# Optimization experiments

Hardware: AMD Instinct MI355X
Metric: run time of the kernel (lower is better)

The kernel has to match this reference:

```python
import jax, jax.numpy as jnp
import numpy as np

N_USERS = 60000
N_ITEMS = 40000
D = 64
N_BEH = 3
L_GLOBAL = 2
L_SINGLE = 2
E_GLOBAL = 1_000_000
E_BEH = 500_000
BATCH = 4096
REG_WEIGHT = 1e-3
DIM_QK = 64
N_NODES = N_USERS + 1 + N_ITEMS + 1
USER_GLOBAL_W = 2.35
USER_BEH_W = 0.242
ITEM_GLOBAL_W = 1.0
ITEM_BEH_W = 0.55


def setup_inputs() -> dict:
    key = jax.random.key(0)
    ks = jax.random.split(key, 9)
    user_emb = (jax.random.normal(ks[0], (N_USERS + 1, D), jnp.float32) * 0.1).at[0].set(0.0)
    item_emb = (jax.random.normal(ks[1], (N_ITEMS + 1, D), jnp.float32) * 0.1).at[0].set(0.0)
    w_scale = 1.0 / np.sqrt(D)
    global_W = jax.random.normal(ks[2], (L_GLOBAL, D, D), jnp.float32) * w_scale
    global_b = jnp.zeros((L_GLOBAL, D), jnp.float32)
    beh_W = jax.random.normal(ks[3], (N_BEH, L_SINGLE, D, D), jnp.float32) * w_scale
    beh_b = jnp.zeros((N_BEH, L_SINGLE, D), jnp.float32)
    all_edge_index = jax.random.randint(ks[4], (2, E_GLOBAL), 0, N_NODES, jnp.int32)
    beh_edge_index = jax.random.randint(ks[5], (N_BEH, 2, E_BEH), 0, N_NODES, jnp.int32)
    batch_data = jax.random.randint(ks[6], (BATCH, N_BEH, 3), 0, N_ITEMS + 1, jnp.int32)
    return {
        "user_emb": user_emb, "item_emb": item_emb,
        "global_W": global_W, "global_b": global_b,
        "beh_W": beh_W, "beh_b": beh_b,
        "all_edge_index": all_edge_index, "beh_edge_index": beh_edge_index,
        "batch_data": batch_data,
    }


def _gcn_conv(h, src, dst, W, b):
    # PyG GCNConv, add_self_loops=False: out[dst] += d^-1/2[src] d^-1/2[dst] (h W)[src] + b
    N = h.shape[0]
    hw = h @ W
    deg = jnp.zeros((N,), hw.dtype).at[dst].add(1.0)
    dinv = jnp.where(deg > 0, jax.lax.rsqrt(jnp.maximum(deg, 1.0)), 0.0)
    coef = (dinv[src] * dinv[dst])[:, None]          # [E,1]
    out = jax.ops.segment_sum(hw[src] * coef, dst, num_segments=N)
    return out + b


def _graph_encoder(x, edge_index, Ws, bs):
    src, dst = edge_index[0], edge_index[1]
    res = x
    h = x
    for i in range(Ws.shape[0]):
        h = _gcn_conv(h, src, dst, Ws[i], bs[i])
        h = h / jnp.maximum(jnp.linalg.norm(h, axis=-1, keepdims=True), 1e-12)  # F.normalize
        res = res + h / (i + 1.0)
    return res


def _mutual_attention(tok):
    # tok: [N, B, D]; per-node BxB softmax attention
    scale = 1.0 / np.sqrt(DIM_QK)
    att = jax.nn.softmax(jnp.einsum('nbd,ncd->nbc', tok, tok) * scale, axis=-1)
    return jnp.einsum('nbc,ncd->nbd', att, tok)


def reference(user_emb, item_emb, global_W, global_b, beh_W, beh_b,
              all_edge_index, beh_edge_index, batch_data):
    nu = user_emb.shape[0]
    all_emb = jnp.concatenate([user_emb, item_emb], axis=0)        # [N, D]
    all_emb = _graph_encoder(all_emb, all_edge_index, global_W, global_b)
    u_g, i_g = all_emb[:nu], all_emb[nu:]
    beh_u, beh_i = [], []
    for b_idx in range(N_BEH):
        e = _graph_encoder(all_emb, beh_edge_index[b_idx], beh_W[b_idx], beh_b[b_idx])
        beh_u.append(e[:nu])
        beh_i.append(e[nu:])
    all_u = jnp.stack(beh_u, axis=1)                               # [nu, B, D]
    all_i = jnp.stack(beh_i, axis=1)                               # [ni, B, D]
    all_u = _mutual_attention(all_u)
    all_i = _mutual_attention(all_i)
    uw = USER_GLOBAL_W * u_g[:, None, :] + USER_BEH_W * all_u      # [nu, B, D]
    iw = ITEM_GLOBAL_W * i_g[:, None, :] + ITEM_BEH_W * all_i      # [ni, B, D]

    total = jnp.float32(0.0)
    for i in range(N_BEH):
        data = batch_data[:, i]
        users = data[:, 0]
        items = data[:, 1:]                                        # [batch, 2]
        uf = uw[:, i][users][:, None, :]                           # [batch, 1, D]
        for j in range(N_BEH):
            itf = iw[:, j][items]                                  # [batch, 2, D]
            scores = jnp.sum(uf * itf, axis=2)                     # [batch, 2]
            total = total - jnp.mean(jax.nn.log_sigmoid(scores[:, 0] - scores[:, 1]))
    emb_loss = (jnp.linalg.norm(user_emb) + jnp.linalg.norm(item_emb)) / item_emb.shape[0]
    return total + REG_WEIGHT * emb_loss
```

## Files before the change

kernel.cpp:

```cpp
#include <hip/hip_runtime.h>
#include <math.h>

#define NU 60001
#define NI 40001
#define NN 100002
#define EG 1000000
#define EB 500000
#define BATCH 4096
#define NPASS 4
#define PASSW 25001
#define EC 36
#define SENTB (NN * 64)

typedef float floatx2 __attribute__((ext_vector_type(2)));
typedef short bf16x8 __attribute__((ext_vector_type(8)));
typedef float f32x4 __attribute__((ext_vector_type(4)));

__device__ inline float wave_sum(float v) {
#pragma unroll
  for (int off = 32; off > 0; off >>= 1) v += __shfl_down(v, off);
  return __shfl(v, 0);
}

__device__ inline float sub_sum16(float v) {
#pragma unroll
  for (int off = 8; off > 0; off >>= 1) v += __shfl_xor(v, off);
  return v;
}

__device__ inline float dot4(float4 a, float4 b) {
  return fmaf(a.x, b.x, fmaf(a.y, b.y, fmaf(a.z, b.z, a.w * b.w)));
}

__device__ inline unsigned short f2b(float f) {
  unsigned u = __float_as_uint(f);
  return (unsigned short)((u + 0x7fffu + ((u >> 16) & 1u)) >> 16);
}
__device__ inline float b2f(unsigned short h) {
  return __uint_as_float((unsigned)h << 16);
}
__device__ inline float4 ld4b(const unsigned short* p) {
  ushort4 u = *(const ushort4*)p;
  return make_float4(b2f(u.x), b2f(u.y), b2f(u.z), b2f(u.w));
}
__device__ inline unsigned pack2b(float a, float b) {
  return (unsigned)f2b(a) | ((unsigned)f2b(b) << 16);
}

__device__ inline unsigned char f2fp8(float f) {
  return (unsigned char)(__builtin_amdgcn_cvt_pk_fp8_f32(f, f, 0, false) & 0xff);
}
__device__ inline unsigned int pack4_fp8(float4 v) {
  int pk = __builtin_amdgcn_cvt_pk_fp8_f32(v.x, v.y, 0, false);
  pk = __builtin_amdgcn_cvt_pk_fp8_f32(v.z, v.w, pk, true);
  return (unsigned int)pk;
}

__global__ void k_bucket(const int* __restrict__ eg, const int* __restrict__ eb,
                         int* __restrict__ cnt, int* __restrict__ edg,
                         int lo, int hi) {
  int set = blockIdx.y;
  int E = set ? EB : EG;
  int e = blockIdx.x * blockDim.x + threadIdx.x;
  if (e >= E) return;
  const int* sp = set ? (eb + (long)(set - 1) * 2 * EB) : eg;
  int d = sp[E + e];
  if (d < lo || d >= hi) return;
  int s = sp[e];
  int pos = atomicAdd(cnt + set * NN + d, 1);
  if (pos < EC) edg[((long)set * NN + d) * EC + pos] = s << 6;
}

__global__ void k_dinv(const int* __restrict__ cnt, float* __restrict__ dinv) {
  int i = blockIdx.x * blockDim.x + threadIdx.x;
  if (i < 4 * NN) {
    int c = cnt[i];
    dinv[i] = (c > 0) ? rsqrtf((float)c) : 0.f;
  }
}

__global__ void k_zsent(unsigned char* __restrict__ tbsb, unsigned char* __restrict__ asg,
                        unsigned char* __restrict__ asb) {
  const long NEp = (long)(NN + 1) * 64;
  int t = threadIdx.x;
  int row = t >> 6, b = t & 63;
  if (row < 3) tbsb[row * NEp + SENTB + b] = 0;
  else if (row == 3) asg[SENTB + b] = 0;
  else if (row < 7) asb[(row - 4) * NEp + SENTB + b] = 0;
}

__global__ void k_tbs0(const float4* __restrict__ ue, const float4* __restrict__ ie,
                       const float* __restrict__ dinv, unsigned int* __restrict__ out) {
  long i = (long)blockIdx.x * blockDim.x + threadIdx.x;
  if (i >= (long)(NN + 1) * 16) return;
  int row = (int)(i >> 4);
  if (row >= NN) { out[i] = 0; return; }
  float4 v = (row < NU) ? ue[i] : ie[i - (long)NU * 16];
  float dv = dinv[row];
  v.x *= dv; v.y *= dv; v.z *= dv; v.w *= dv;
  out[i] = pack4_fp8(v);
}

template <int MODE>
__global__ void __launch_bounds__(256) k_gcn(
    const unsigned char* __restrict__ tb, const int* __restrict__ edg,
    const int* __restrict__ cnt, const float* __restrict__ dinv,
    const float* __restrict__ Wb, const float* __restrict__ biasb,
    const float* __restrict__ basef, const float* __restrict__ base2f,
    const unsigned short* __restrict__ base16,
    unsigned short* __restrict__ res16, unsigned char* __restrict__ outS,
    unsigned char* __restrict__ tbs123) {
  __shared__ __align__(16) short accs[32][72];
  __shared__ float ssq[32][2];
  const long NE = (long)NN * 64;
  const long NEp = (long)(NN + 1) * 64;

  int t = threadIdx.x;
  int w = t >> 6, lane = t & 63;
  int sub3 = lane >> 3, sl8 = lane & 7;
  int sub = lane >> 4, sl16 = lane & 15;
  int set = blockIdx.y;

  const float *W, *bias;
  if (MODE <= 1) { W = Wb; bias = biasb; }
  else {
    W = Wb + (long)set * 8192 + (MODE == 3 ? 4096 : 0);
    bias = biasb + set * 128 + (MODE == 3 ? 64 : 0);
  }
  int cs = (MODE >= 2) ? (1 + set) : 0;
  const unsigned char* tbl = (MODE >= 2) ? tb + (long)set * NEp : tb;
  unsigned char* outp = (MODE == 2) ? outS + (long)set * NEp : outS;

  int tilebase = (w >> 1) << 4;
  int cg = (w & 1) << 5;
  int ncolA = cg + sl16, ncolB = cg + 16 + sl16;
  bf16x8 bfA0, bfA1, bfB0, bfB1;
#pragma unroll
  for (int j = 0; j < 8; j++) {
    int k0 = (sub * 8 + j) * 64, k1 = (32 + sub * 8 + j) * 64;
    bfA0[j] = (short)f2b(W[k0 + ncolA]);
    bfA1[j] = (short)f2b(W[k1 + ncolA]);
    bfB0[j] = (short)f2b(W[k0 + ncolB]);
    bfB1[j] = (short)f2b(W[k1 + ncolB]);
  }
  float biasA = bias[ncolA], biasB = bias[ncolB];

  int nb0 = blockIdx.x * 32;
  int node = nb0 + (w << 3) + sub3;
  floatx2 a0 = {0.f, 0.f}, a1 = {0.f, 0.f}, a2 = {0.f, 0.f}, a3 = {0.f, 0.f};
  int deg = 0;
  float dvn = 0.f;
  const int* ep = edg;
  if (node < NN) {
    deg = min(cnt[cs * NN + node], EC);
    dvn = dinv[cs * NN + node];
    ep = edg + ((long)cs * NN + node) * EC;
  }
  int mx = deg;
  mx = max(mx, __shfl_xor(mx, 8));
  mx = max(mx, __shfl_xor(mx, 16));
  mx = max(mx, __shfl_xor(mx, 32));
  int lb = lane & 56;
  for (int ch = 0; ch < mx; ch += 8) {
    int rem = deg - ch;
    int e = (sl8 < rem) ? ep[ch + sl8] : 0;
#pragma unroll
    for (int i = 0; i < 8; i += 4) {
      int s0 = __shfl(e, lb + i),     s1 = __shfl(e, lb + i + 1);
      int s2 = __shfl(e, lb + i + 2), s3 = __shfl(e, lb + i + 3);
      int o0 = (i + 0 < rem) ? s0 : SENTB;
      int o1 = (i + 1 < rem) ? s1 : SENTB;
      int o2 = (i + 2 < rem) ? s2 : SENTB;
      int o3 = (i + 3 < rem) ? s3 : SENTB;
      uint2 r0 = *(const uint2*)(tbl + o0 + (sl8 << 3));
      uint2 r1 = *(const uint2*)(tbl + o1 + (sl8 << 3));
      uint2 r2 = *(const uint2*)(tbl + o2 + (sl8 << 3));
      uint2 r3 = *(const uint2*)(tbl + o3 + (sl8 << 3));
      a0 += __builtin_amdgcn_cvt_pk_f32_fp8(r0.x, false);
      a1 += __builtin_amdgcn_cvt_pk_f32_fp8(r0.x, true);
      a2 += __builtin_amdgcn_cvt_pk_f32_fp8(r0.y, false);
      a3 += __builtin_amdgcn_cvt_pk_f32_fp8(r0.y, true);
      a0 += __builtin_amdgcn_cvt_pk_f32_fp8(r1.x, false);
      a1 += __builtin_amdgcn_cvt_pk_f32_fp8(r1.x, true);
      a2 += __builtin_amdgcn_cvt_pk_f32_fp8(r1.y, false);
      a3 += __builtin_amdgcn_cvt_pk_f32_fp8(r1.y, true);
      a0 += __builtin_amdgcn_cvt_pk_f32_fp8(r2.x, false);
      a1 += __builtin_amdgcn_cvt_pk_f32_fp8(r2.x, true);
      a2 += __builtin_amdgcn_cvt_pk_f32_fp8(r2.y, false);
      a3 += __builtin_amdgcn_cvt_pk_f32_fp8(r2.y, true);
      a0 += __builtin_amdgcn_cvt_pk_f32_fp8(r3.x, false);
      a1 += __builtin_amdgcn_cvt_pk_f32_fp8(r3.x, true);
      a2 += __builtin_amdgcn_cvt_pk_f32_fp8(r3.y, false);
      a3 += __builtin_amdgcn_cvt_pk_f32_fp8(r3.y, true);
    }
  }
  floatx2 dv2 = {dvn, dvn};
  a0 *= dv2; a1 *= dv2; a2 *= dv2; a3 *= dv2;
  int4 pk4;
  pk4.x = (int)pack2b(a0.x, a0.y);
  pk4.y = (int)pack2b(a1.x, a1.y);
  pk4.z = (int)pack2b(a2.x, a2.y);
  pk4.w = (int)pack2b(a3.x, a3.y);
  *(int4*)&accs[(w << 3) + sub3][sl8 << 3] = pk4;
  __syncthreads();

  int arow = tilebase + sl16;
  bf16x8 fa0 = *(const bf16x8*)&accs[arow][sub << 3];
  bf16x8 fa1 = *(const bf16x8*)&accs[arow][32 + (sub << 3)];
  f32x4 cA = {0.f, 0.f, 0.f, 0.f}, cB = {0.f, 0.f, 0.f, 0.f};
  cA = __builtin_amdgcn_mfma_f32_16x16x32_bf16(fa0, bfA0, cA, 0, 0, 0);
  cA = __builtin_amdgcn_mfma_f32_16x16x32_bf16(fa1, bfA1, cA, 0, 0, 0);
  cB = __builtin_amdgcn_mfma_f32_16x16x32_bf16(fa0, bfB0, cB, 0, 0, 0);
  cB = __builtin_amdgcn_mfma_f32_16x16x32_bf16(fa1, bfB1, cB, 0, 0, 0);

  float vA[4], vB[4];
#pragma unroll
  for (int r = 0; r < 4; r++) { vA[r] = cA[r] + biasA; vB[r] = cB[r] + biasB; }
#pragma unroll
  for (int r = 0; r < 4; r++) {
    float p = sub_sum16(fmaf(vA[r], vA[r], vB[r] * vB[r]));
    if (sl16 == 0) ssq[tilebase + (sub << 2) + r][w & 1] = p;
  }
  __syncthreads();
#pragma unroll
  for (int r = 0; r < 4; r++) {
    int nl = tilebase + (sub << 2) + r;
    float ss = ssq[nl][0] + ssq[nl][1];
    float inv = 1.0f / fmaxf(sqrtf(ss), 1e-12f);
    float hA = vA[r] * inv, hB = vB[r] * inv;
    int gn = nb0 + nl;
    if (gn < NN) {
      long iA = (long)gn * 64 + ncolA, iB = (long)gn * 64 + ncolB;
      float dv = dinv[cs * NN + gn];
      if (MODE == 0 || MODE == 2) {
        outp[iA] = f2fp8(hA * dv);
        outp[iB] = f2fp8(hB * dv);
      } else if (MODE == 1) {
        float idv = (dv > 0.f) ? 1.0f / dv : 0.f;
        float ownA = __builtin_amdgcn_cvt_f32_fp8((unsigned int)tbl[iA], 0) * idv;
        float ownB = __builtin_amdgcn_cvt_f32_fp8((unsigned int)tbl[iB], 0) * idv;
        float bA, bB;
        if (gn < NU) { bA = basef[iA]; bB = basef[iB]; }
        else {
          long o2 = (long)(gn - NU) * 64;
          bA = base2f[o2 + ncolA]; bB = base2f[o2 + ncolB];
        }
        float rA = bA + ownA + 0.5f * hA, rB = bB + ownB + 0.5f * hB;
        res16[iA] = f2b(rA); res16[iB] = f2b(rB);
#pragma unroll
        for (int k = 0; k < 3; k++) {
          float dk = dinv[(1 + k) * NN + gn];
          tbs123[(long)k * NEp + iA] = f2fp8(rA * dk);
          tbs123[(long)k * NEp + iB] = f2fp8(rB * dk);
        }
      } else {
        float idv = (dv > 0.f) ? 1.0f / dv : 0.f;
        float ownA = __builtin_amdgcn_cvt_f32_fp8((unsigned int)tbl[iA], 0) * idv;
        float ownB = __builtin_amdgcn_cvt_f32_fp8((unsigned int)tbl[iB], 0) * idv;
        float rA = b2f(base16[iA]) + ownA + 0.5f * hA;
        float rB = b2f(base16[iB]) + ownB + 0.5f * hB;
        (res16 + (long)set * NE)[iA] = f2b(rA);
        (res16 + (long)set * NE)[iB] = f2b(rB);
      }
    }
  }
}

__device__ inline void item_iw4(const unsigned short* __restrict__ G,
                                const unsigned short* __restrict__ B0,
                                const unsigned short* __restrict__ B1,
                                const unsigned short* __restrict__ B2,
                                long o, float4& iw0, float4& iw1, float4& iw2) {
  float4 g = ld4b(G + o);
  float4 t0 = ld4b(B0 + o);
  float4 t1 = ld4b(B1 + o);
  float4 t2 = ld4b(B2 + o);
  float g00 = sub_sum16(dot4(t0, t0)), g01 = sub_sum16(dot4(t0, t1));
  float g02 = sub_sum16(dot4(t0, t2)), g11 = sub_sum16(dot4(t1, t1));
  float g12 = sub_sum16(dot4(t1, t2)), g22 = sub_sum16(dot4(t2, t2));
  const float S = 0.125f;
  float gm[3][3] = {{g00, g01, g02}, {g01, g11, g12}, {g02, g12, g22}};
  float4* out[3] = {&iw0, &iw1, &iw2};
#pragma unroll
  for (int j = 0; j < 3; j++) {
    float a0 = gm[j][0] * S, a1 = gm[j][1] * S, a2 = gm[j][2] * S;
    float m = fmaxf(a0, fmaxf(a1, a2));
    float e0 = expf(a0 - m), e1 = expf(a1 - m), e2 = expf(a2 - m);
    float inv = 1.f / (e0 + e1 + e2);
    float w0 = e0 * inv, w1 = e1 * inv, w2 = e2 * inv;
    float4 r;
    r.x = fmaf(0.55f, w0 * t0.x + w1 * t1.x + w2 * t2.x, g.x);
    r.y = fmaf(0.55f, w0 * t0.y + w1 * t1.y + w2 * t2.y, g.y);
    r.z = fmaf(0.55f, w0 * t0.z + w1 * t1.z + w2 * t2.z, g.z);
    r.w = fmaf(0.55f, w0 * t0.w + w1 * t1.w + w2 * t2.w, g.w);
    *out[j] = r;
  }
}

__global__ void __launch_bounds__(256) k_loss(
    const unsigned short* __restrict__ G, const unsigned short* __restrict__ B0,
    const unsigned short* __restrict__ B1, const unsigned short* __restrict__ B2,
    const int* __restrict__ batch, float* __restrict__ acc) {
  int tid = blockIdx.x * blockDim.x + threadIdx.x;
  int lane = tid & 63;
  int sub = lane >> 4, sl = lane & 15;
  int task = (tid >> 6) * 4 + sub;
  if (task >= BATCH * 3) return;
  int i = task % 3;
  const int* bd = batch + (long)task * 3;
  int u = bd[0], p = bd[1], q = bd[2];

  float4 uf;
  {
    long o = (long)u * 64 + sl * 4;
    float4 g = ld4b(G + o);
    float4 t0 = ld4b(B0 + o);
    float4 t1 = ld4b(B1 + o);
    float4 t2 = ld4b(B2 + o);
    float4 ti = (i == 0) ? t0 : ((i == 1) ? t1 : t2);
    float a0 = sub_sum16(dot4(ti, t0)) * 0.125f;
    float a1 = sub_sum16(dot4(ti, t1)) * 0.125f;
    float a2 = sub_sum16(dot4(ti, t2)) * 0.125f;
    float m = fmaxf(a0, fmaxf(a1, a2));
    float e0 = expf(a0 - m), e1 = expf(a1 - m), e2 = expf(a2 - m);
    float inv = 1.f / (e0 + e1 + e2);
    float w0 = e0 * inv, w1 = e1 * inv, w2 = e2 * inv;
    uf.x = fmaf(2.35f, g.x, 0.242f * (w0 * t0.x + w1 * t1.x + w2 * t2.x));
    uf.y = fmaf(2.35f, g.y, 0.242f * (w0 * t0.y + w1 * t1.y + w2 * t2.y));
    uf.z = fmaf(2.35f, g.z, 0.242f * (w0 * t0.z + w1 * t1.z + w2 * t2.z));
    uf.w = fmaf(2.35f, g.w, 0.242f * (w0 * t0.w + w1 * t1.w + w2 * t2.w));
  }

  float4 p0, p1, p2, q0, q1, q2;
  item_iw4(G, B0, B1, B2, ((long)(NU + p)) * 64 + sl * 4, p0, p1, p2);
  item_iw4(G, B0, B1, B2, ((long)(NU + q)) * 64 + sl * 4, q0, q1, q2);

  float sp0 = sub_sum16(dot4(uf, p0)), sq0 = sub_sum16(dot4(uf, q0));
  float sp1 = sub_sum16(dot4(uf, p1)), sq1 = sub_sum16(dot4(uf, q1));
  float sp2 = sub_sum16(dot4(uf, p2)), sq2 = sub_sum16(dot4(uf, q2));

  if (sl == 0) {
    float loc = 0.f;
    float xs[3] = {sp0 - sq0, sp1 - sq1, sp2 - sq2};
#pragma unroll
    for (int j = 0; j < 3; j++) {
      float x = xs[j];
      loc += fminf(x, 0.f) - log1pf(expf(-fabsf(x)));
    }
    atomicAdd(acc, loc);
  }
}

__global__ void k_sumsq(const float* __restrict__ x, long n, float* __restrict__ acc) {
  long stride = (long)gridDim.x * blockDim.x;
  float v = 0.f;
  for (long i = (long)blockIdx.x * blockDim.x + threadIdx.x; i < n; i += stride) {
    float t = x[i];
    v = fmaf(t, t, v);
  }
  v = wave_sum(v);
  if ((threadIdx.x & 63) == 0) atomicAdd(acc, v);
}

__global__ void k_final(const float* __restrict__ acc, float* __restrict__ out) {
  out[0] = -acc[0] * (1.0f / (float)BATCH) +
           0.001f * ((sqrtf(acc[1]) + sqrtf(acc[2])) / (float)NI);
}

extern "C" void kernel_launch(void* const* d_in, const int* in_sizes, int n_in,
                              void* d_out, int out_size, void* d_ws, size_t ws_size,
                              hipStream_t stream) {
  const float* ue = (const float*)d_in[0];
  const float* ie = (const float*)d_in[1];
  const float* gW = (const float*)d_in[2];
  const float* gb = (const float*)d_in[3];
  const float* bW = (const float*)d_in[4];
  const float* bb = (const float*)d_in[5];
  const int* eg = (const int*)d_in[6];
  const int* eb = (const int*)d_in[7];
  const int* batch = (const int*)d_in[8];
  float* out = (float*)d_out;

  const long NE = (long)NN * 64;
  const long NEp = (long)(NN + 1) * 64;
  unsigned short* G16 = (unsigned short*)d_ws;
  unsigned short* B16 = G16 + NE;
  float* DINV = (float*)(B16 + 3 * NE);
  float* ACC = DINV + 4 * NN;
  int* CNT = (int*)(ACC + 8);
  int* EDG = CNT + 4 * NN;
  unsigned char* TBS0 = (unsigned char*)(EDG + 4L * NN * EC);
  unsigned char* TBSb = TBS0 + NEp;
  unsigned char* ASg = TBSb + 3 * NEp;
  unsigned char* ASb = ASg + NEp;

  hipMemsetAsync(ACC, 0, 8 * sizeof(float), stream);
  hipMemsetAsync(CNT, 0, 4 * NN * sizeof(int), stream);

  const int GB = (NN + 31) / 32;

  dim3 ge((EG + 255) / 256, 4);

  for (int p = 0; p < NPASS; p++)
    k_bucket<<<ge, 256, 0, stream>>>(eg, eb, CNT, EDG,
                                     p * PASSW, min(NN, (p + 1) * PASSW));
  k_dinv<<<(4 * NN + 255) / 256, 256, 0, stream>>>(CNT, DINV);
  k_zsent<<<1, 512, 0, stream>>>(TBSb, ASg, ASb);
  k_tbs0<<<(int)(((NN + 1) * 16 + 255) / 256), 256, 0, stream>>>(
      (const float4*)ue, (const float4*)ie, DINV, (unsigned int*)TBS0);

  k_gcn<0><<<dim3(GB, 1), 256, 0, stream>>>(TBS0, EDG, CNT, DINV, gW, gb,
                                            nullptr, nullptr, nullptr, nullptr,
                                            ASg, nullptr);
  k_gcn<1><<<dim3(GB, 1), 256, 0, stream>>>(ASg, EDG, CNT, DINV, gW + 4096, gb + 64,
                                            ue, ie, nullptr, G16, nullptr, TBSb);

  k_gcn<2><<<dim3(GB, 3), 256, 0, stream>>>(TBSb, EDG, CNT, DINV, bW, bb,
                                            nullptr, nullptr, nullptr, nullptr,
                                            ASb, nullptr);
  k_gcn<3><<<dim3(GB, 3), 256, 0, stream>>>(ASb, EDG, CNT, DINV, bW, bb,
                                            nullptr, nullptr, G16, B16, nullptr,
                                            nullptr);

  k_loss<<<(BATCH * 3) / 16, 256, 0, stream>>>(G16, B16, B16 + NE, B16 + 2 * NE,
                                               batch, ACC);

  k_sumsq<<<512, 256, 0, stream>>>(ue, (long)NU * 64, ACC + 1);
  k_sumsq<<<512, 256, 0, stream>>>(ie, (long)NI * 64, ACC + 2);

  k_final<<<1, 1, 0, stream>>>(ACC, out);
}
```

Before: 548.2 us.

## Sort nodes by degree for load-balanced GCN gather and pre-transpose weights

Adds a histogram, scan and scatter pass that builds a per-graph permutation of nodes ordered by in-degree. The GCN kernels then process nodes in that order, so each wave's eight nodes have similar degree, which cuts the divergence and idle lanes in the edge gather loop. A fast unguarded loop covers the chunks shared by all nodes in the wave. Weights are also converted once into transposed bf16 so each block loads its MFMA fragments with vector loads. The cost is extra small kernel launches and scattered output writes, since neighbouring permuted nodes are no longer adjacent in memory.

Result: slower. 625.1 us (+14.0%).

```diff
diff --git a/kernel.cpp b/kernel.cpp
--- a/kernel.cpp
+++ b/kernel.cpp
@@ -10,6 +10,7 @@
 #define NPASS 4
 #define PASSW 25001
 #define EC 36
+#define NBIN 40
 #define SENTB (NN * 64)
 
 typedef float floatx2 __attribute__((ext_vector_type(2)));
@@ -79,6 +80,75 @@
   }
 }
 
+__global__ void k_hist(const int* __restrict__ cnt, int* __restrict__ hist) {
+  __shared__ int lh[NBIN];
+  int set = blockIdx.y;
+  int t = threadIdx.x;
+  if (t < NBIN) lh[t] = 0;
+  __syncthreads();
+  int base = blockIdx.x * 1024;
+#pragma unroll
+  for (int j = 0; j < 4; j++) {
+    int n = base + t + j * 256;
+    if (n < NN) {
+      int b = min(cnt[set * NN + n], EC);
+      atomicAdd(&lh[b], 1);
+    }
+  }
+  __syncthreads();
+  if (t < NBIN && lh[t]) atomicAdd(&hist[set * NBIN + t], lh[t]);
+}
+
+__global__ void k_scan(const int* __restrict__ hist, int* __restrict__ hbase) {
+  int s = threadIdx.x;
+  if (s < 4) {
+    int acc = 0;
+    for (int b = 0; b < NBIN; b++) {
+      hbase[s * NBIN + b] = acc;
+      acc += hist[s * NBIN + b];
+    }
+  }
+}
+
+__global__ void k_scatter(const int* __restrict__ cnt, int* __restrict__ hbase,
+                          int* __restrict__ perm) {
+  __shared__ int lh[NBIN], gb[NBIN];
+  int set = blockIdx.y;
+  int t = threadIdx.x;
+  if (t < NBIN) lh[t] = 0;
+  __syncthreads();
+  int base = blockIdx.x * 1024;
+  int myb[4], myr[4];
+#pragma unroll
+  for (int j = 0; j < 4; j++) {
+    int n = base + t + j * 256;
+    myb[j] = -1;
+    if (n < NN) {
+      int b = min(cnt[set * NN + n], EC);
+      myb[j] = b;
+      myr[j] = atomicAdd(&lh[b], 1);
+    }
+  }
+  __syncthreads();
+  if (t < NBIN) gb[t] = lh[t] ? atomicAdd(&hbase[set * NBIN + t], lh[t]) : 0;
+  __syncthreads();
+#pragma unroll
+  for (int j = 0; j < 4; j++) {
+    if (myb[j] >= 0)
+      perm[(long)set * NN + gb[myb[j]] + myr[j]] = base + t + j * 256;
+  }
+}
+
+__global__ void k_prepw(const float* __restrict__ gW, const float* __restrict__ bW,
+                        unsigned short* __restrict__ wt) {
+  int t = blockIdx.x * blockDim.x + threadIdx.x;
+  if (t >= 8 * 4096) return;
+  int m = t >> 12, idx = t & 4095;
+  int col = idx >> 6, k = idx & 63;
+  const float* src = (m < 2) ? (gW + m * 4096) : (bW + (long)(m - 2) * 4096);
+  wt[t] = f2b(src[k * 64 + col]);
+}
+
 __global__ void k_zsent(unsigned char* __restrict__ tbsb, unsigned char* __restrict__ asg,
                         unsigned char* __restrict__ asb) {
   const long NEp = (long)(NN + 1) * 64;
@@ -101,11 +171,18 @@
   out[i] = pack4_fp8(v);
 }
 
+#define CVT8(r)                                       \
+  a0 += __builtin_amdgcn_cvt_pk_f32_fp8(r.x, false);  \
+  a1 += __builtin_amdgcn_cvt_pk_f32_fp8(r.x, true);   \
+  a2 += __builtin_amdgcn_cvt_pk_f32_fp8(r.y, false);  \
+  a3 += __builtin_amdgcn_cvt_pk_f32_fp8(r.y, true);
+
 template <int MODE>
 __global__ void __launch_bounds__(256) k_gcn(
     const unsigned char* __restrict__ tb, const int* __restrict__ edg,
     const int* __restrict__ cnt, const float* __restrict__ dinv,
-    const float* __restrict__ Wb, const float* __restrict__ biasb,
+    const int* __restrict__ perm, const unsigned short* __restrict__ Wt,
+    const float* __restrict__ biasb,
     const float* __restrict__ basef, const float* __restrict__ base2f,
     const unsigned short* __restrict__ base16,
     unsigned short* __restrict__ res16, unsigned char* __restrict__ outS,
@@ -121,32 +198,27 @@
   int sub = lane >> 4, sl16 = lane & 15;
   int set = blockIdx.y;
 
-  const float *W, *bias;
-  if (MODE <= 1) { W = Wb; bias = biasb; }
-  else {
-    W = Wb + (long)set * 8192 + (MODE == 3 ? 4096 : 0);
-    bias = biasb + set * 128 + (MODE == 3 ? 64 : 0);
-  }
+  const float* bias;
+  if (MODE <= 1) bias = biasb;
+  else bias = biasb + set * 128 + (MODE == 3 ? 64 : 0);
+  const unsigned short* wt = Wt + ((MODE >= 2) ? (long)set * 8192 : 0);
   int cs = (MODE >= 2) ? (1 + set) : 0;
   const unsigned char* tbl = (MODE >= 2) ? tb + (long)set * NEp : tb;
   unsigned char* outp = (MODE == 2) ? outS + (long)set * NEp : outS;
+  const int* pp = perm + (long)cs * NN;
 
   int tilebase = (w >> 1) << 4;
   int cg = (w & 1) << 5;
   int ncolA = cg + sl16, ncolB = cg + 16 + sl16;
-  bf16x8 bfA0, bfA1, bfB0, bfB1;
-#pragma unroll
-  for (int j = 0; j < 8; j++) {
-    int k0 = (sub * 8 + j) * 64, k1 = (32 + sub * 8 + j) * 64;
-    bfA0[j] = (short)f2b(W[k0 + ncolA]);
-    bfA1[j] = (short)f2b(W[k1 + ncolA]);
-    bfB0[j] = (short)f2b(W[k0 + ncolB]);
-    bfB1[j] = (short)f2b(W[k1 + ncolB]);
-  }
+  bf16x8 bfA0 = *(const bf16x8*)(wt + ncolA * 64 + (sub << 3));
+  bf16x8 bfA1 = *(const bf16x8*)(wt + ncolA * 64 + 32 + (sub << 3));
+  bf16x8 bfB0 = *(const bf16x8*)(wt + ncolB * 64 + (sub << 3));
+  bf16x8 bfB1 = *(const bf16x8*)(wt + ncolB * 64 + 32 + (sub << 3));
   float biasA = bias[ncolA], biasB = bias[ncolB];
 
   int nb0 = blockIdx.x * 32;
-  int node = nb0 + (w << 3) + sub3;
+  int idx = nb0 + (w << 3) + sub3;
+  int node = (idx < NN) ? pp[idx] : NN;
   floatx2 a0 = {0.f, 0.f}, a1 = {0.f, 0.f}, a2 = {0.f, 0.f}, a3 = {0.f, 0.f};
   int deg = 0;
   float dvn = 0.f;
@@ -156,12 +228,29 @@
     dvn = dinv[cs * NN + node];
     ep = edg + ((long)cs * NN + node) * EC;
   }
-  int mx = deg;
+  int mx = deg, mn = deg;
   mx = max(mx, __shfl_xor(mx, 8));
   mx = max(mx, __shfl_xor(mx, 16));
   mx = max(mx, __shfl_xor(mx, 32));
+  mn = min(mn, __shfl_xor(mn, 8));
+  mn = min(mn, __shfl_xor(mn, 16));
+  mn = min(mn, __shfl_xor(mn, 32));
+  int mnf = mn & ~7;
   int lb = lane & 56;
-  for (int ch = 0; ch < mx; ch += 8) {
+  for (int ch = 0; ch < mnf; ch += 8) {
+    int e = ep[ch + sl8];
+#pragma unroll
+    for (int i = 0; i < 8; i += 4) {
+      int o0 = __shfl(e, lb + i),     o1 = __shfl(e, lb + i + 1);
+      int o2 = __shfl(e, lb + i + 2), o3 = __shfl(e, lb + i + 3);
+      uint2 r0 = *(const uint2*)(tbl + o0 + (sl8 << 3));
+      uint2 r1 = *(const uint2*)(tbl + o1 + (sl8 << 3));
+      uint2 r2 = *(const uint2*)(tbl + o2 + (sl8 << 3));
+      uint2 r3 = *(const uint2*)(tbl + o3 + (sl8 << 3));
+      CVT8(r0); CVT8(r1); CVT8(r2); CVT8(r3);
+    }
+  }
+  for (int ch = mnf; ch < mx; ch += 8) {
     int rem = deg - ch;
     int e = (sl8 < rem) ? ep[ch + sl8] : 0;
 #pragma unroll
@@ -176,22 +265,7 @@
       uint2 r1 = *(const uint2*)(tbl + o1 + (sl8 << 3));
       uint2 r2 = *(const uint2*)(tbl + o2 + (sl8 << 3));
       uint2 r3 = *(const uint2*)(tbl + o3 + (sl8 << 3));
-      a0 += __builtin_amdgcn_cvt_pk_f32_fp8(r0.x, false);
-      a1 += __builtin_amdgcn_cvt_pk_f32_fp8(r0.x, true);
-      a2 += __builtin_amdgcn_cvt_pk_f32_fp8(r0.y, false);
-      a3 += __builtin_amdgcn_cvt_pk_f32_fp8(r0.y, true);
-      a0 += __builtin_amdgcn_cvt_pk_f32_fp8(r1.x, false);
-      a1 += __builtin_amdgcn_cvt_pk_f32_fp8(r1.x, true);
-      a2 += __builtin_amdgcn_cvt_pk_f32_fp8(r1.y, false);
-      a3 += __builtin_amdgcn_cvt_pk_f32_fp8(r1.y, true);
-      a0 += __builtin_amdgcn_cvt_pk_f32_fp8(r2.x, false);
-      a1 += __builtin_amdgcn_cvt_pk_f32_fp8(r2.x, true);
-      a2 += __builtin_amdgcn_cvt_pk_f32_fp8(r2.y, false);
-      a3 += __builtin_amdgcn_cvt_pk_f32_fp8(r2.y, true);
-      a0 += __builtin_amdgcn_cvt_pk_f32_fp8(r3.x, false);
-      a1 += __builtin_amdgcn_cvt_pk_f32_fp8(r3.x, true);
-      a2 += __builtin_amdgcn_cvt_pk_f32_fp8(r3.y, false);
-      a3 += __builtin_amdgcn_cvt_pk_f32_fp8(r3.y, true);
+      CVT8(r0); CVT8(r1); CVT8(r2); CVT8(r3);
     }
   }
   floatx2 dv2 = {dvn, dvn};
@@ -228,8 +302,9 @@
     float ss = ssq[nl][0] + ssq[nl][1];
     float inv = 1.0f / fmaxf(sqrtf(ss), 1e-12f);
     float hA = vA[r] * inv, hB = vB[r] * inv;
-    int gn = nb0 + nl;
-    if (gn < NN) {
+    int il = nb0 + nl;
+    if (il < NN) {
+      int gn = pp[il];
       long iA = (long)gn * 64 + ncolA, iB = (long)gn * 64 + ncolB;
       float dv = dinv[cs * NN + gn];
       if (MODE == 0 || MODE == 2) {
@@ -388,16 +463,21 @@
   float* DINV = (float*)(B16 + 3 * NE);
   float* ACC = DINV + 4 * NN;
   int* CNT = (int*)(ACC + 8);
-  int* EDG = CNT + 4 * NN;
+  int* HIST = CNT + 4 * NN;
+  int* HBASE = HIST + 4 * NBIN;
+  int* PERM = HBASE + 4 * NBIN;
+  unsigned short* WT = (unsigned short*)(PERM + 4 * NN);
+  int* EDG = (int*)(WT + 8 * 4096);
   unsigned char* TBS0 = (unsigned char*)(EDG + 4L * NN * EC);
   unsigned char* TBSb = TBS0 + NEp;
   unsigned char* ASg = TBSb + 3 * NEp;
   unsigned char* ASb = ASg + NEp;
 
   hipMemsetAsync(ACC, 0, 8 * sizeof(float), stream);
-  hipMemsetAsync(CNT, 0, 4 * NN * sizeof(int), stream);
+  hipMemsetAsync(CNT, 0, (4 * NN + 4 * NBIN) * sizeof(int), stream);
 
   const int GB = (NN + 31) / 32;
+  const int SB = (NN + 1023) / 1024;
 
   dim3 ge((EG + 255) / 256, 4);
 
@@ -405,22 +485,30 @@
     k_bucket<<<ge, 256, 0, stream>>>(eg, eb, CNT, EDG,
                                      p * PASSW, min(NN, (p + 1) * PASSW));
   k_dinv<<<(4 * NN + 255) / 256, 256, 0, stream>>>(CNT, DINV);
+
+  k_hist<<<dim3(SB, 4), 256, 0, stream>>>(CNT, HIST);
+  k_scan<<<1, 64, 0, stream>>>(HIST, HBASE);
+  k_scatter<<<dim3(SB, 4), 256, 0, stream>>>(CNT, HBASE, PERM);
+
+  k_prepw<<<128, 256, 0, stream>>>(gW, bW, WT);
+
   k_zsent<<<1, 512, 0, stream>>>(TBSb, ASg, ASb);
   k_tbs0<<<(int)(((NN + 1) * 16 + 255) / 256), 256, 0, stream>>>(
       (const float4*)ue, (const float4*)ie, DINV, (unsigned int*)TBS0);
 
-  k_gcn<0><<<dim3(GB, 1), 256, 0, stream>>>(TBS0, EDG, CNT, DINV, gW, gb,
+  k_gcn<0><<<dim3(GB, 1), 256, 0, stream>>>(TBS0, EDG, CNT, DINV, PERM, WT, gb,
                                             nullptr, nullptr, nullptr, nullptr,
                                             ASg, nullptr);
-  k_gcn<1><<<dim3(GB, 1), 256, 0, stream>>>(ASg, EDG, CNT, DINV, gW + 4096, gb + 64,
-                                            ue, ie, nullptr, G16, nullptr, TBSb);
-
-  k_gcn<2><<<dim3(GB, 3), 256, 0, stream>>>(TBSb, EDG, CNT, DINV, bW, bb,
-                                            nullptr, nullptr, nullptr, nullptr,
-                                            ASb, nullptr);
-  k_gcn<3><<<dim3(GB, 3), 256, 0, stream>>>(ASb, EDG, CNT, DINV, bW, bb,
-                                            nullptr, nullptr, G16, B16, nullptr,
-                                            nullptr);
+  k_gcn<1><<<dim3(GB, 1), 256, 0, stream>>>(ASg, EDG, CNT, DINV, PERM, WT + 4096,
+                                            gb + 64, ue, ie, nullptr, G16,
+                                            nullptr, TBSb);
+
+  k_gcn<2><<<dim3(GB, 3), 256, 0, stream>>>(TBSb, EDG, CNT, DINV, PERM, WT + 8192,
+                                            bb, nullptr, nullptr, nullptr,
+                                            nullptr, ASb, nullptr);
+  k_gcn<3><<<dim3(GB, 3), 256, 0, stream>>>(ASb, EDG, CNT, DINV, PERM, WT + 12288,
+                                            bb, nullptr, nullptr, G16, B16,
+                                            nullptr, nullptr);
 
   k_loss<<<(BATCH * 3) / 16, 256, 0, stream>>>(G16, B16, B16 + NE, B16 + 2 * NE,
                                                batch, ACC);
```
